# Performance work log

Measured on AMD Instinct MI355X. Metric: run time of the kernel, lower is better.

Reference implementation:

```python
import jax, jax.numpy as jnp
import numpy as np

# longformer-base-4096 config
L, H, D, DH, FF = 12, 12, 768, 64, 3072
B, S, W = 1, 4096, 256            # W = one-sided attention window (attention_window 512)
V, MAXP, NCLS = 50265, 4098, 6
NC = S // W                        # number of chunks of size W


def layer_norm(x, s, b, eps=1e-5):
    m = jnp.mean(x, -1, keepdims=True)
    v = jnp.var(x, -1, keepdims=True)
    return (x - m) * jax.lax.rsqrt(v + eps) * s + b


def sliding_attn(q, k, v, kv_mask):
    # q,k,v: [B,H,S,DH]; kv_mask: [B,S] float (1=keep, 0=pad)
    qc = q.reshape(B, H, NC, W, DH)
    pad = ((0, 0), (0, 0), (W, W), (0, 0))
    kp = jnp.pad(k, pad).reshape(B, H, NC + 2, W, DH)
    vp = jnp.pad(v, pad).reshape(B, H, NC + 2, W, DH)
    # each chunk c sees key chunks c-1, c, c+1 -> [B,H,NC,3W,DH]
    k3 = jnp.concatenate([kp[:, :, i:i + NC] for i in range(3)], axis=3)
    v3 = jnp.concatenate([vp[:, :, i:i + NC] for i in range(3)], axis=3)
    scores = jnp.einsum('bhcqd,bhckd->bhcqk', qc, k3) / np.float32(np.sqrt(DH))
    # banded mask: |key_global - query_global| <= W  <=>  qi <= kj <= qi + 2W
    qi = jnp.arange(W)[:, None]
    kj = jnp.arange(3 * W)[None, :]
    band = (kj >= qi) & (kj <= qi + 2 * W)                       # [W,3W]
    mp = jnp.pad(kv_mask, ((0, 0), (W, W))).reshape(B, NC + 2, W)
    m3 = jnp.concatenate([mp[:, i:i + NC] for i in range(3)], axis=2)  # [B,NC,3W]
    allowed = band[None, None, None] & (m3[:, None, :, None, :] > 0)
    probs = jax.nn.softmax(jnp.where(allowed, scores, -1e9), axis=-1)
    out = jnp.einsum('bhcqk,bhckd->bhcqd', probs, v3)            # [B,H,NC,W,DH]
    return out.reshape(B, H, S, DH)


def setup_inputs():
    ki = iter(jax.random.split(jax.random.key(0), 16))
    p = lambda sh: 0.02 * jax.random.normal(next(ki), sh, jnp.float32)
    ids = jax.random.randint(next(ki), (B, S), 0, V, dtype=jnp.int32)
    mask = jnp.ones((B, S), jnp.int32)
    return dict(
        ids=ids, mask=mask,
        word_emb=p((V, D)), pos_emb=p((MAXP, D)), type_emb=p((D,)),
        ln_e_s=jnp.ones((D,), jnp.float32), ln_e_b=jnp.zeros((D,), jnp.float32),
        wq=p((L, D, D)), bq=jnp.zeros((L, D), jnp.float32),
        wk=p((L, D, D)), bk=jnp.zeros((L, D), jnp.float32),
        wv=p((L, D, D)), bv=jnp.zeros((L, D), jnp.float32),
        wo=p((L, D, D)), bo=jnp.zeros((L, D), jnp.float32),
        ln1_s=jnp.ones((L, D), jnp.float32), ln1_b=jnp.zeros((L, D), jnp.float32),
        w1=p((L, D, FF)), b1=jnp.zeros((L, FF), jnp.float32),
        w2=p((L, FF, D)), b2=jnp.zeros((L, D), jnp.float32),
        ln2_s=jnp.ones((L, D), jnp.float32), ln2_b=jnp.zeros((L, D), jnp.float32),
        w_pool=p((D, D)), b_pool=jnp.zeros((D,), jnp.float32),
        w_cls=p((D, NCLS)), b_cls=jnp.zeros((NCLS,), jnp.float32))


def reference(ids, mask, word_emb, pos_emb, type_emb, ln_e_s, ln_e_b,
              wq, bq, wk, bk, wv, bv, wo, bo, ln1_s, ln1_b,
              w1, b1, w2, b2, ln2_s, ln2_b, w_pool, b_pool, w_cls, b_cls):
    maskf = mask.astype(jnp.float32)
    # RoBERTa-style position ids with padding_idx=1
    pos = (jnp.cumsum(mask, axis=1) * mask + 1).astype(jnp.int32)
    x = word_emb[ids] + pos_emb[pos] + type_emb               # [B,S,D]
    x = layer_norm(x, ln_e_s, ln_e_b)

    def heads(y, w, b):
        return (y @ w + b).reshape(B, S, H, DH).transpose(0, 2, 1, 3)

    for l in range(L):
        q = heads(x, wq[l], bq[l])
        k = heads(x, wk[l], bk[l])
        v = heads(x, wv[l], bv[l])
        a = sliding_attn(q, k, v, maskf)                      # [B,H,S,DH]
        a = a.transpose(0, 2, 1, 3).reshape(B, S, D)
        x = layer_norm(x + (a @ wo[l] + bo[l]), ln1_s[l], ln1_b[l])
        h = jax.nn.gelu(x @ w1[l] + b1[l], approximate=False)
        x = layer_norm(x + (h @ w2[l] + b2[l]), ln2_s[l], ln2_b[l])

    pooled = jnp.tanh(x[:, 0] @ w_pool + b_pool)              # [B,D] pooler
    # Dropout(0.3) is identity in eval mode
    return pooled @ w_cls + b_cls                             # [B,6]
```

## Files before the change

kernel.cpp:

```cpp
#include <hip/hip_runtime.h>
#include <stdint.h>
#include <math.h>

#define NL 12
#define SQ 4096
#define DM 768
#define NH 12
#define DHD 64
#define FF 3072
#define WW 256

typedef unsigned short u16;
typedef __attribute__((ext_vector_type(8))) short bf8_t;
typedef __attribute__((ext_vector_type(4))) short s16x4;
typedef __attribute__((ext_vector_type(4))) float f4;

__device__ __forceinline__ float bf2f(u16 h) {
  union { unsigned int u; float f; } c; c.u = ((unsigned int)h) << 16; return c.f;
}
__device__ __forceinline__ u16 f2bf(float f) {
  union { float f; unsigned int u; } c; c.f = f; unsigned int u = c.u;
  return (u16)((u + 0x7fffu + ((u >> 16) & 1u)) >> 16);
}
__device__ __forceinline__ int iclamp(int v, int lo, int hi) {
  return v < lo ? lo : (v > hi ? hi : v);
}
__device__ __forceinline__ void gload16(const void* g, void* l) {
  __builtin_amdgcn_global_load_lds(
      (const __attribute__((address_space(1))) void*)g,
      (__attribute__((address_space(3))) void*)l, 16, 0, 0);
}

__global__ __launch_bounds__(256) void scan_kernel(const int* __restrict__ mask,
                                                   int* __restrict__ pos) {
  __shared__ int part[256];
  int tid = threadIdx.x;
  int base = tid * 16, ssum = 0;
  for (int i = 0; i < 16; ++i) ssum += mask[base + i];
  part[tid] = ssum;
  __syncthreads();
  if (tid == 0) {
    int run = 0;
    for (int i = 0; i < 256; ++i) { int t = part[i]; part[i] = run; run += t; }
  }
  __syncthreads();
  int run = part[tid];
  for (int i = 0; i < 16; ++i) {
    int m = mask[base + i];
    run += m;
    pos[base + i] = run * m + 1;
  }
}

__device__ __forceinline__ void block_ln4(int row, f4 a, bool act,
    const float* __restrict__ s, const float* __restrict__ b,
    float* __restrict__ xo, u16* __restrict__ xh, float* red, int tid) {
  float s1 = 0.f, s2 = 0.f;
  if (act) {
#pragma unroll
    for (int j = 0; j < 4; ++j) { s1 += a[j]; s2 += a[j] * a[j]; }
  }
#pragma unroll
  for (int m = 1; m < 64; m <<= 1) { s1 += __shfl_xor(s1, m); s2 += __shfl_xor(s2, m); }
  if ((tid & 63) == 0) { red[tid >> 6] = s1; red[4 + (tid >> 6)] = s2; }
  __syncthreads();
  s1 = red[0] + red[1] + red[2] + red[3];
  s2 = red[4] + red[5] + red[6] + red[7];
  float mean = s1 * (1.f / DM);
  float var = s2 * (1.f / DM) - mean * mean;
  float inv = rsqrtf(var + 1e-5f);
  if (act) {
    const f4 sv = ((const f4*)s)[tid];
    const f4 bv = ((const f4*)b)[tid];
    f4 y;
    s16x4 hh;
#pragma unroll
    for (int j = 0; j < 4; ++j) {
      y[j] = (a[j] - mean) * inv * sv[j] + bv[j];
      hh[j] = (short)f2bf(y[j]);
    }
    ((f4*)xo)[(size_t)row * 192 + tid] = y;
    *(s16x4*)&xh[(size_t)row * DM + tid * 4] = hh;
  }
}

__global__ __launch_bounds__(256) void embed_kernel(const int* __restrict__ ids,
    const int* __restrict__ pos, const float* __restrict__ we,
    const float* __restrict__ pe, const float* __restrict__ te,
    const float* __restrict__ s, const float* __restrict__ b,
    float* __restrict__ xo, u16* __restrict__ xh) {
  __shared__ float red[8];
  int row = blockIdx.x, tid = threadIdx.x;
  bool act = tid < 192;
  f4 a = { 0.f, 0.f, 0.f, 0.f };
  if (act) {
    int id = ids[row], pz = pos[row];
    const f4 wv = ((const f4*)we)[(size_t)id * 192 + tid];
    const f4 pv = ((const f4*)pe)[(size_t)pz * 192 + tid];
    const f4 tv = ((const f4*)te)[tid];
#pragma unroll
    for (int j = 0; j < 4; ++j) a[j] = wv[j] + pv[j] + tv[j];
  }
  block_ln4(row, a, act, s, b, xo, xh, red, tid);
}

__global__ __launch_bounds__(256) void ln_direct_kernel(
    const float* __restrict__ in, float* __restrict__ x, u16* __restrict__ xh,
    const float* __restrict__ s, const float* __restrict__ b) {
  __shared__ float red[8];
  int row = blockIdx.x, tid = threadIdx.x;
  bool act = tid < 192;
  f4 a = { 0.f, 0.f, 0.f, 0.f };
  if (act) a = ((const f4*)in)[(size_t)row * 192 + tid];
  block_ln4(row, a, act, s, b, x, xh, red, tid);
}

__global__ __launch_bounds__(256) void ln_fuse_kernel(
    const float* __restrict__ pp, int nparts, const float* __restrict__ bias,
    float* __restrict__ x, u16* __restrict__ xh,
    const float* __restrict__ s, const float* __restrict__ b) {
  __shared__ float red[8];
  int row = blockIdx.x, tid = threadIdx.x;
  bool act = tid < 192;
  f4 a = { 0.f, 0.f, 0.f, 0.f };
  if (act) {
    size_t i4 = (size_t)row * 192 + tid;
    a = ((const f4*)x)[i4];
    const f4 bb = ((const f4*)bias)[tid];
#pragma unroll
    for (int j = 0; j < 4; ++j) a[j] += bb[j];
    for (int p = 0; p < nparts; ++p) {
      const f4 pv = ((const f4*)pp)[(size_t)p * SQ * 192 + i4];
#pragma unroll
      for (int j = 0; j < 4; ++j) a[j] += pv[j];
    }
  }
  block_ln4(row, a, act, s, b, x, xh, red, tid);
}

__global__ __launch_bounds__(256) void wconv_all(
    const float* __restrict__ wq, const float* __restrict__ wk,
    const float* __restrict__ wv, const float* __restrict__ wo,
    const float* __restrict__ w1, const float* __restrict__ w2,
    u16* __restrict__ Wqkv, u16* __restrict__ Wo,
    u16* __restrict__ W1, u16* __restrict__ W2) {
  __shared__ float t[64 * 65];
  int b = blockIdx.x;
  int lay = blockIdx.y;
  const float* src;
  u16* dst;
  int K, N, rowoff, nx, tile;
  if (b < 216) {
    int j = b / 72;
    tile = b - j * 72;
    src = ((j == 0) ? wq : ((j == 1) ? wk : wv)) + (size_t)lay * DM * DM;
    dst = Wqkv + (size_t)lay * 3 * DM * DM;
    K = DM; N = DM; rowoff = j * DM; nx = 12;
  } else if (b < 288) {
    tile = b - 216;
    src = wo + (size_t)lay * DM * DM; dst = Wo + (size_t)lay * DM * DM;
    K = DM; N = DM; rowoff = 0; nx = 12;
  } else if (b < 576) {
    tile = b - 288;
    src = w1 + (size_t)lay * DM * FF; dst = W1 + (size_t)lay * DM * FF;
    K = DM; N = FF; rowoff = 0; nx = 48;
  } else {
    tile = b - 576;
    src = w2 + (size_t)lay * FF * DM; dst = W2 + (size_t)lay * FF * DM;
    K = FF; N = DM; rowoff = 0; nx = 12;
  }
  int n0 = (tile % nx) * 64, k0 = (tile / nx) * 128;
  int tid = threadIdx.x;
  int q = tid & 15, kr = tid >> 4;

  f4 v0[4], v1[4];
#pragma unroll
  for (int p = 0; p < 4; ++p)
    v0[p] = *(const f4*)&src[(size_t)(k0 + kr + p * 16) * N + n0 + q * 4];
#pragma unroll
  for (int p = 0; p < 4; ++p)
    v1[p] = *(const f4*)&src[(size_t)(k0 + 64 + kr + p * 16) * N + n0 + q * 4];

#pragma unroll
  for (int p = 0; p < 4; ++p) {
    int k = kr + p * 16;
#pragma unroll
    for (int j = 0; j < 4; ++j) t[k * 65 + q * 4 + j] = v0[p][j];
  }
  __syncthreads();
  {
    int n = tid >> 4, kq = (tid & 15) * 4;
#pragma unroll
    for (int c = 0; c < 4; ++c) {
      int nn = n + c * 16;
      s16x4 st;
#pragma unroll
      for (int i = 0; i < 4; ++i)
        st[i] = (short)f2bf(t[(kq + i) * 65 + nn]);
      *(s16x4*)&dst[(size_t)(rowoff + n0 + nn) * K + k0 + kq] = st;
    }
  }
  __syncthreads();
#pragma unroll
  for (int p = 0; p < 4; ++p) {
    int k = kr + p * 16;
#pragma unroll
    for (int j = 0; j < 4; ++j) t[k * 65 + q * 4 + j] = v1[p][j];
  }
  __syncthreads();
  {
    int n = tid >> 4, kq = (tid & 15) * 4;
#pragma unroll
    for (int c = 0; c < 4; ++c) {
      int nn = n + c * 16;
      s16x4 st;
#pragma unroll
      for (int i = 0; i < 4; ++i)
        st[i] = (short)f2bf(t[(kq + i) * 65 + nn]);
      *(s16x4*)&dst[(size_t)(rowoff + n0 + nn) * K + k0 + 64 + kq] = st;
    }
  }
}

template <int EPI>
__global__ __launch_bounds__(256, 3) void gemm1(
    const u16* __restrict__ A, const u16* __restrict__ B, int Kld, int ksl,
    int nx, int ntiles,
    const float* __restrict__ bias0, const float* __restrict__ bias1,
    const float* __restrict__ bias2, const float* __restrict__ resid,
    float* __restrict__ outf, u16* __restrict__ oh,
    u16* __restrict__ Qb, u16* __restrict__ Kb, u16* __restrict__ VTb) {
  __shared__ __align__(16) char smem[49152];

  const int tid = threadIdx.x;
  const int l = tid & 63;
  const int w = tid >> 6;
  const int lr = l & 15;
  const int lg = l >> 4;
  const int nwg = gridDim.x;
  const int bid = blockIdx.x;
  const int wg = (bid & 7) * (nwg >> 3) + (bid >> 3);
  const int part = wg / ntiles;
  const int t = wg - part * ntiles;
  const int bm = (t / nx) * 128;
  const int bn = (t % nx) * 64;
  const int k0 = part * ksl;
  const int wr = (w >> 1) * 64;
  const int wc = (w & 1) * 32;

  f4 acc[4][2];
  f4 z = { 0.f, 0.f, 0.f, 0.f };
#pragma unroll
  for (int i = 0; i < 4; ++i)
#pragma unroll
    for (int j = 0; j < 2; ++j) acc[i][j] = z;

  const int srow = tid >> 3;
  const int scol = ((tid & 7) * 8) ^ ((srow & 7) * 8);
  const int xw = (lr & 7) * 8;

  const int nkt = ksl >> 6;

  auto stage = [&](int slot, int kt) {
    int ksrc = k0 + (kt << 6);
    char* la = smem + slot * 24576 + (size_t)(tid & ~63) * 16;
    char* lb = la + 16384;
#pragma unroll
    for (int r = 0; r < 4; ++r)
      gload16(A + (size_t)(bm + srow + r * 32) * Kld + ksrc + scol, la + r * 4096);
#pragma unroll
    for (int r = 0; r < 2; ++r)
      gload16(B + (size_t)(bn + srow + r * 32) * Kld + ksrc + scol, lb + r * 4096);
  };

  stage(0, 0);
  stage(1, 1);
  asm volatile("s_waitcnt vmcnt(6)" ::: "memory");
  __builtin_amdgcn_s_barrier();
  __builtin_amdgcn_sched_barrier(0);

  for (int kt = 0; kt < nkt; ++kt) {
    const int cur = kt & 1;
    const u16* sA = (const u16*)(smem + cur * 24576);
    const u16* sB = sA + 8192;
#pragma unroll
    for (int ks = 0; ks < 2; ++ks) {
      bf8_t af[4], bfr[2];
#pragma unroll
      for (int mt = 0; mt < 4; ++mt)
        af[mt] = *(const bf8_t*)&sA[(wr + mt * 16 + lr) * 64 + ((ks * 32 + lg * 8) ^ xw)];
#pragma unroll
      for (int nt = 0; nt < 2; ++nt)
        bfr[nt] = *(const bf8_t*)&sB[(wc + nt * 16 + lr) * 64 + ((ks * 32 + lg * 8) ^ xw)];
#pragma unroll
      for (int mt = 0; mt < 4; ++mt)
#pragma unroll
        for (int nt = 0; nt < 2; ++nt)
          acc[mt][nt] = __builtin_amdgcn_mfma_f32_16x16x32_bf16(af[mt], bfr[nt], acc[mt][nt], 0, 0, 0);
    }
    asm volatile("s_waitcnt lgkmcnt(0)" ::: "memory");
    __builtin_amdgcn_sched_barrier(0);
    __builtin_amdgcn_s_barrier();
    if (kt + 2 < nkt) {
      stage(cur, kt + 2);
      asm volatile("s_waitcnt vmcnt(6)" ::: "memory");
    } else {
      asm volatile("s_waitcnt vmcnt(0)" ::: "memory");
    }
    __builtin_amdgcn_s_barrier();
    __builtin_amdgcn_sched_barrier(0);
  }
  __syncthreads();

  if constexpr (EPI == 3 || EPI == 4) {
#pragma unroll
    for (int mt = 0; mt < 4; ++mt)
#pragma unroll
      for (int nt = 0; nt < 2; ++nt) {
        int colg = bn + wc + nt * 16 + lr;
#pragma unroll
        for (int r = 0; r < 4; ++r) {
          int rowg = bm + wr + mt * 16 + lg * 4 + r;
          size_t idx = (size_t)rowg * DM + colg;
          if constexpr (EPI == 3) {
            outf[(size_t)part * SQ * DM + idx] = acc[mt][nt][r];
          } else {
            outf[idx] = acc[mt][nt][r] + bias0[colg] + resid[idx];
          }
        }
      }
    return;
  }

  float* ep = (float*)(smem + w * 9216);
  const int nbase = bn + wc;

  if constexpr (EPI == 0) {
    int tgt = nbase / DM;
    int within = nbase - tgt * DM;
    int head = within >> 6;
    const float* bp = (tgt == 0) ? bias0 : ((tgt == 1) ? bias1 : bias2);
    if (tgt == 2) {
#pragma unroll
      for (int mt = 0; mt < 4; ++mt)
#pragma unroll
        for (int nt = 0; nt < 2; ++nt) {
          int dh = (within & 63) + nt * 16 + lr;
          float bb = bp[within + nt * 16 + lr];
          int s0 = bm + wr + mt * 16 + lg * 4;
          s16x4 st;
#pragma unroll
          for (int r = 0; r < 4; ++r) st[r] = (short)f2bf(acc[mt][nt][r] + bb);
          *(s16x4*)&VTb[((size_t)(head * DHD + dh)) * SQ + s0] = st;
        }
    } else {
      u16* dst = (tgt == 0) ? Qb : Kb;
      float scale = (tgt == 0) ? 0.125f : 1.0f;
#pragma unroll
      for (int mt = 0; mt < 4; ++mt)
#pragma unroll
        for (int nt = 0; nt < 2; ++nt)
#pragma unroll
          for (int r = 0; r < 4; ++r)
            ep[(mt * 16 + lg * 4 + r) * 36 + nt * 16 + lr] = acc[mt][nt][r];
      asm volatile("s_waitcnt lgkmcnt(0)" ::: "memory");
      int coloff = (l & 7) * 4;
#pragma unroll
      for (int i = 0; i < 8; ++i) {
        int row = (l >> 3) + i * 8;
        int gs = bm + wr + row;
        f4 v = *(f4*)&ep[row * 36 + coloff];
        s16x4 st;
#pragma unroll
        for (int j = 0; j < 4; ++j)
          st[j] = (short)f2bf((v[j] + bp[within + coloff + j]) * scale);
        *(s16x4*)&dst[((size_t)head * SQ + gs) * DHD + (within & 63) + coloff] = st;
      }
    }
  } else {
#pragma unroll
    for (int mt = 0; mt < 4; ++mt)
#pragma unroll
      for (int nt = 0; nt < 2; ++nt)
#pragma unroll
        for (int r = 0; r < 4; ++r)
          ep[(mt * 16 + lg * 4 + r) * 36 + nt * 16 + lr] = acc[mt][nt][r];
    asm volatile("s_waitcnt lgkmcnt(0)" ::: "memory");
    int coloff = (l & 7) * 4;
#pragma unroll
    for (int i = 0; i < 8; ++i) {
      int row = (l >> 3) + i * 8;
      int gs = bm + wr + row;
      f4 v = *(f4*)&ep[row * 36 + coloff];
      s16x4 hi;
#pragma unroll
      for (int j = 0; j < 4; ++j) {
        float t2 = v[j] + bias0[nbase + coloff + j];
        t2 = 0.5f * t2 * (1.f + erff(t2 * 0.70710678118654752f));
        hi[j] = (short)f2bf(t2);
      }
      *(s16x4*)&oh[(size_t)gs * FF + nbase + coloff] = hi;
    }
  }
}

__global__ __launch_bounds__(64) void attn_kernel(
    const u16* __restrict__ Qb, const u16* __restrict__ Kb,
    const u16* __restrict__ VTb, const int* __restrict__ mask,
    u16* __restrict__ ah) {
  __shared__ __align__(16) u16 Pl[64 * 72];
  __shared__ float mwin[576];
  const int l = threadIdx.x;
  const int lr = l & 15, lg = l >> 4;
  const int h = blockIdx.y;
  const int q0 = blockIdx.x * 64;
  const int kb = q0 - 256;
  for (int i = l; i < 576; i += 64) {
    int kg = kb + i;
    mwin[i] = (kg >= 0 && kg < SQ && mask[kg] != 0) ? 1.f : 0.f;
  }
  __syncthreads();

  bf8_t qf[4][2];
#pragma unroll
  for (int mt = 0; mt < 4; ++mt)
#pragma unroll
    for (int ks = 0; ks < 2; ++ks)
      qf[mt][ks] = *(const bf8_t*)&Qb[((size_t)h * SQ + q0 + mt * 16 + lr) * DHD + ks * 32 + lg * 8];

  f4 o[4][4];
  f4 z = { 0.f, 0.f, 0.f, 0.f };
  float mrow[4][4], lrow[4][4];
#pragma unroll
  for (int mt = 0; mt < 4; ++mt)
#pragma unroll
    for (int nt = 0; nt < 4; ++nt) o[mt][nt] = z;
#pragma unroll
  for (int mt = 0; mt < 4; ++mt)
#pragma unroll
    for (int r = 0; r < 4; ++r) { mrow[mt][r] = -1e30f; lrow[mt][r] = 0.f; }

  for (int kc = 0; kc < 9; ++kc) {
    int klb = kc * 64;
    f4 sc[4][4];
#pragma unroll
    for (int mt = 0; mt < 4; ++mt)
#pragma unroll
      for (int nt = 0; nt < 4; ++nt) sc[mt][nt] = z;
#pragma unroll
    for (int ks = 0; ks < 2; ++ks) {
      bf8_t kf[4];
#pragma unroll
      for (int nt = 0; nt < 4; ++nt) {
        int krow = iclamp(kb + klb + nt * 16 + lr, 0, SQ - 1);
        kf[nt] = *(const bf8_t*)&Kb[((size_t)h * SQ + krow) * DHD + ks * 32 + lg * 8];
      }
#pragma unroll
      for (int mt = 0; mt < 4; ++mt)
#pragma unroll
        for (int nt = 0; nt < 4; ++nt)
          sc[mt][nt] = __builtin_amdgcn_mfma_f32_16x16x32_bf16(qf[mt][ks], kf[nt], sc[mt][nt], 0, 0, 0);
    }
    bool edge = (kc == 0) | (kc == 8);
#pragma unroll
    for (int mt = 0; mt < 4; ++mt)
#pragma unroll
      for (int nt = 0; nt < 4; ++nt) {
        int col = nt * 16 + lr;
        int kg = kb + klb + col;
        float mk = mwin[klb + col];
#pragma unroll
        for (int r = 0; r < 4; ++r) {
          int qg = q0 + mt * 16 + lg * 4 + r;
          int d = kg - qg;
          bool ok = (mk > 0.5f) && (!edge || ((d <= WW) && (d >= -WW)));
          sc[mt][nt][r] = ok ? sc[mt][nt][r] : -3.0e38f;
        }
      }
#pragma unroll
    for (int mt = 0; mt < 4; ++mt)
#pragma unroll
      for (int r = 0; r < 4; ++r) {
        float cm = fmaxf(fmaxf(sc[mt][0][r], sc[mt][1][r]),
                         fmaxf(sc[mt][2][r], sc[mt][3][r]));
#pragma unroll
        for (int m2 = 1; m2 < 16; m2 <<= 1) cm = fmaxf(cm, __shfl_xor(cm, m2));
        float mn = fmaxf(fmaxf(mrow[mt][r], cm), -1e30f);
        float scl = __expf(mrow[mt][r] - mn);
        mrow[mt][r] = mn;
        float ps = 0.f;
#pragma unroll
        for (int nt = 0; nt < 4; ++nt) {
          float pv = __expf(sc[mt][nt][r] - mn);
          sc[mt][nt][r] = pv;
          ps += pv;
        }
#pragma unroll
        for (int m2 = 1; m2 < 16; m2 <<= 1) ps += __shfl_xor(ps, m2);
        lrow[mt][r] = lrow[mt][r] * scl + ps;
#pragma unroll
        for (int nt = 0; nt < 4; ++nt) o[mt][nt][r] *= scl;
#pragma unroll
        for (int nt = 0; nt < 4; ++nt)
          Pl[(mt * 16 + lg * 4 + r) * 72 + nt * 16 + lr] = f2bf(sc[mt][nt][r]);
      }
    asm volatile("s_waitcnt lgkmcnt(0)" ::: "memory");
#pragma unroll
    for (int ks = 0; ks < 2; ++ks) {
      bf8_t pa[4], vf[4];
#pragma unroll
      for (int mt = 0; mt < 4; ++mt)
        pa[mt] = *(const bf8_t*)&Pl[(mt * 16 + lr) * 72 + ks * 32 + lg * 8];
      int kbase = iclamp(kb + klb + ks * 32 + lg * 8, 0, SQ - 8);
#pragma unroll
      for (int nt = 0; nt < 4; ++nt)
        vf[nt] = *(const bf8_t*)&VTb[((size_t)h * DHD + nt * 16 + lr) * SQ + kbase];
#pragma unroll
      for (int mt = 0; mt < 4; ++mt)
#pragma unroll
        for (int nt = 0; nt < 4; ++nt)
          o[mt][nt] = __builtin_amdgcn_mfma_f32_16x16x32_bf16(pa[mt], vf[nt], o[mt][nt], 0, 0, 0);
    }
  }
#pragma unroll
  for (int mt = 0; mt < 4; ++mt)
#pragma unroll
    for (int nt = 0; nt < 4; ++nt) {
      int col = h * DHD + nt * 16 + lr;
#pragma unroll
      for (int r = 0; r < 4; ++r) {
        int gq = q0 + mt * 16 + lg * 4 + r;
        float v = o[mt][nt][r] / lrow[mt][r];
        ah[(size_t)gq * DM + col] = f2bf(v);
      }
    }
}

__global__ __launch_bounds__(256) void head1_kernel(const float* __restrict__ x,
    const float* __restrict__ wp, const float* __restrict__ bp,
    float* __restrict__ y) {
  __shared__ float x0[DM];
  __shared__ float part[4][64];
  int tid = threadIdx.x;
  int w = tid >> 6, l = tid & 63;
  for (int i = tid; i < DM; i += 256) x0[i] = x[i];
  __syncthreads();
  int j = blockIdx.x * 64 + l;
  float a = 0.f;
  int i0 = w * 192;
#pragma unroll 4
  for (int i = i0; i < i0 + 192; ++i) a += x0[i] * wp[(size_t)i * DM + j];
  part[w][l] = a;
  __syncthreads();
  if (w == 0) {
    float t = part[0][l] + part[1][l] + part[2][l] + part[3][l] + bp[j];
    y[j] = tanhf(t);
  }
}

__global__ __launch_bounds__(64) void head2_kernel(const float* __restrict__ y,
    const float* __restrict__ wc, const float* __restrict__ bc,
    float* __restrict__ out) {
  int l = threadIdx.x;
  float acc[6] = {0.f, 0.f, 0.f, 0.f, 0.f, 0.f};
  for (int i = l; i < DM; i += 64) {
    float yv = y[i];
#pragma unroll
    for (int j = 0; j < 6; ++j) acc[j] += yv * wc[i * 6 + j];
  }
#pragma unroll
  for (int j = 0; j < 6; ++j)
#pragma unroll
    for (int m = 1; m < 64; m <<= 1) acc[j] += __shfl_xor(acc[j], m);
  if (l == 0) {
#pragma unroll
    for (int j = 0; j < 6; ++j) out[j] = acc[j] + bc[j];
  }
}

extern "C" void kernel_launch(void* const* d_in, const int* in_sizes, int n_in,
                              void* d_out, int out_size, void* d_ws, size_t ws_size,
                              hipStream_t stream) {
  const int* ids = (const int*)d_in[0];
  const int* mask = (const int*)d_in[1];
  const float* we = (const float*)d_in[2];
  const float* pe = (const float*)d_in[3];
  const float* te = (const float*)d_in[4];
  const float* ln_e_s = (const float*)d_in[5];
  const float* ln_e_b = (const float*)d_in[6];
  const float* wq = (const float*)d_in[7];
  const float* bq = (const float*)d_in[8];
  const float* wk = (const float*)d_in[9];
  const float* bk = (const float*)d_in[10];
  const float* wv = (const float*)d_in[11];
  const float* bv = (const float*)d_in[12];
  const float* wo = (const float*)d_in[13];
  const float* bo = (const float*)d_in[14];
  const float* ln1_s = (const float*)d_in[15];
  const float* ln1_b = (const float*)d_in[16];
  const float* w1 = (const float*)d_in[17];
  const float* b1 = (const float*)d_in[18];
  const float* w2 = (const float*)d_in[19];
  const float* b2 = (const float*)d_in[20];
  const float* ln2_s = (const float*)d_in[21];
  const float* ln2_b = (const float*)d_in[22];
  const float* wpool = (const float*)d_in[23];
  const float* bpool = (const float*)d_in[24];
  const float* wcls = (const float*)d_in[25];
  const float* bcls = (const float*)d_in[26];

  char* p = (char*)d_ws;
  auto take = [&](size_t bytes) {
    char* r = p;
    p += (bytes + 255) & ~(size_t)255;
    return r;
  };
  int* pos = (int*)take((size_t)SQ * 4);
  float* x = (float*)take((size_t)SQ * DM * 4);
  float* pp = (float*)take((size_t)2 * SQ * DM * 4);
  u16* xh = (u16*)take((size_t)SQ * DM * 2);
  u16* Wqkv_h = (u16*)take((size_t)NL * 3 * DM * DM * 2);
  u16* Wo_h = (u16*)take((size_t)NL * DM * DM * 2);
  u16* W1_h = (u16*)take((size_t)NL * DM * FF * 2);
  u16* W2_h = (u16*)take((size_t)NL * FF * DM * 2);
  u16* Qb = (u16*)take((size_t)NH * SQ * DHD * 2);
  u16* Kbf = (u16*)take((size_t)NH * SQ * DHD * 2);
  u16* VTb = (u16*)take((size_t)NH * DHD * SQ * 2);
  u16* ah_ = (u16*)take((size_t)SQ * DM * 2);
  u16* hh = (u16*)take((size_t)SQ * FF * 2);
  float* ypool = (float*)take((size_t)DM * 4);

  scan_kernel<<<dim3(1), dim3(256), 0, stream>>>(mask, pos);
  embed_kernel<<<dim3(SQ), dim3(256), 0, stream>>>(ids, pos, we, pe, te, ln_e_s, ln_e_b, x, xh);
  wconv_all<<<dim3(864, NL), dim3(256), 0, stream>>>(
      wq, wk, wv, wo, w1, w2, Wqkv_h, Wo_h, W1_h, W2_h);

  for (int l = 0; l < NL; ++l) {
    const u16* Wq_l = Wqkv_h + (size_t)l * 3 * DM * DM;
    const u16* Wo_l = Wo_h + (size_t)l * DM * DM;
    const u16* W1_l = W1_h + (size_t)l * DM * FF;
    const u16* W2_l = W2_h + (size_t)l * FF * DM;

    gemm1<0><<<dim3(1152), dim3(256), 0, stream>>>(
        xh, Wq_l, DM, DM, 36, 1152, bq + (size_t)l * DM, bk + (size_t)l * DM,
        bv + (size_t)l * DM, nullptr, nullptr, nullptr, Qb, Kbf, VTb);
    attn_kernel<<<dim3(SQ / 64, NH), dim3(64), 0, stream>>>(Qb, Kbf, VTb, mask, ah_);
    gemm1<4><<<dim3(384), dim3(256), 0, stream>>>(
        ah_, Wo_l, DM, DM, 12, 384, bo + (size_t)l * DM, nullptr, nullptr, x,
        pp, nullptr, nullptr, nullptr, nullptr);
    ln_direct_kernel<<<dim3(SQ), dim3(256), 0, stream>>>(
        pp, x, xh, ln1_s + (size_t)l * DM, ln1_b + (size_t)l * DM);
    gemm1<2><<<dim3(1536), dim3(256), 0, stream>>>(
        xh, W1_l, DM, DM, 48, 1536, b1 + (size_t)l * FF, nullptr, nullptr, nullptr,
        nullptr, hh, nullptr, nullptr, nullptr);
    gemm1<3><<<dim3(768), dim3(256), 0, stream>>>(
        hh, W2_l, FF, FF / 2, 12, 384, nullptr, nullptr, nullptr, nullptr,
        pp, nullptr, nullptr, nullptr, nullptr);
    ln_fuse_kernel<<<dim3(SQ), dim3(256), 0, stream>>>(
        pp, 2, b2 + (size_t)l * DM, x, xh, ln2_s + (size_t)l * DM, ln2_b + (size_t)l * DM);
  }

  head1_kernel<<<dim3(12), dim3(256), 0, stream>>>(x, wpool, bpool, ypool);
  head2_kernel<<<dim3(1), dim3(64), 0, stream>>>(ypool, wcls, bcls, (float*)d_out);
}
```

Before: 2.239 ms.

## Split attention block into two waves of 32 queries and skip mask when fully valid

The attention kernel now launches 128 threads per block, and each of the two waves handles 32 query rows over its own 576-key window. Each wave has a private P staging buffer in LDS, and the mask window is widened to 640 entries. Per-wave register use drops (accumulators and scores are halved), and a ballot over the mask window lets non-edge chunks skip the per-element masking when every key is valid. In exchange, each wave loads its own K/V tiles, so global and L2 traffic for K and V roughly doubles, and the MFMA work per key load goes down.

```diff
diff --git a/kernel.cpp b/kernel.cpp
--- a/kernel.cpp
+++ b/kernel.cpp
@@ -404,47 +404,52 @@
   }
 }
 
-__global__ __launch_bounds__(64) void attn_kernel(
+__global__ __launch_bounds__(128) void attn_kernel(
     const u16* __restrict__ Qb, const u16* __restrict__ Kb,
     const u16* __restrict__ VTb, const int* __restrict__ mask,
     u16* __restrict__ ah) {
-  __shared__ __align__(16) u16 Pl[64 * 72];
-  __shared__ float mwin[576];
-  const int l = threadIdx.x;
+  __shared__ __align__(16) u16 Pl[2][32 * 72];
+  __shared__ float mwin[640];
+  const int tid = threadIdx.x;
+  const int w = tid >> 6;
+  const int l = tid & 63;
   const int lr = l & 15, lg = l >> 4;
   const int h = blockIdx.y;
   const int q0 = blockIdx.x * 64;
-  const int kb = q0 - 256;
-  for (int i = l; i < 576; i += 64) {
-    int kg = kb + i;
+  const int qw = q0 + w * 32;
+  const int kbw = qw - 256;
+  for (int i = tid; i < 640; i += 128) {
+    int kg = q0 - 256 + i;
     mwin[i] = (kg >= 0 && kg < SQ && mask[kg] != 0) ? 1.f : 0.f;
   }
   __syncthreads();
-
-  bf8_t qf[4][2];
-#pragma unroll
-  for (int mt = 0; mt < 4; ++mt)
+  u16* Plw = Pl[w];
+
+  bf8_t qf[2][2];
+#pragma unroll
+  for (int mt = 0; mt < 2; ++mt)
 #pragma unroll
     for (int ks = 0; ks < 2; ++ks)
-      qf[mt][ks] = *(const bf8_t*)&Qb[((size_t)h * SQ + q0 + mt * 16 + lr) * DHD + ks * 32 + lg * 8];
-
-  f4 o[4][4];
+      qf[mt][ks] = *(const bf8_t*)&Qb[((size_t)h * SQ + qw + mt * 16 + lr) * DHD + ks * 32 + lg * 8];
+
+  f4 o[2][4];
   f4 z = { 0.f, 0.f, 0.f, 0.f };
-  float mrow[4][4], lrow[4][4];
-#pragma unroll
-  for (int mt = 0; mt < 4; ++mt)
+  float mrow[2][4], lrow[2][4];
+#pragma unroll
+  for (int mt = 0; mt < 2; ++mt)
 #pragma unroll
     for (int nt = 0; nt < 4; ++nt) o[mt][nt] = z;
 #pragma unroll
-  for (int mt = 0; mt < 4; ++mt)
+  for (int mt = 0; mt < 2; ++mt)
 #pragma unroll
     for (int r = 0; r < 4; ++r) { mrow[mt][r] = -1e30f; lrow[mt][r] = 0.f; }
 
   for (int kc = 0; kc < 9; ++kc) {
     int klb = kc * 64;
-    f4 sc[4][4];
-#pragma unroll
-    for (int mt = 0; mt < 4; ++mt)
+    int mo = w * 32 + klb;
+    f4 sc[2][4];
+#pragma unroll
+    for (int mt = 0; mt < 2; ++mt)
 #pragma unroll
       for (int nt = 0; nt < 4; ++nt) sc[mt][nt] = z;
 #pragma unroll
@@ -452,33 +457,36 @@
       bf8_t kf[4];
 #pragma unroll
       for (int nt = 0; nt < 4; ++nt) {
-        int krow = iclamp(kb + klb + nt * 16 + lr, 0, SQ - 1);
+        int krow = iclamp(kbw + klb + nt * 16 + lr, 0, SQ - 1);
         kf[nt] = *(const bf8_t*)&Kb[((size_t)h * SQ + krow) * DHD + ks * 32 + lg * 8];
       }
 #pragma unroll
-      for (int mt = 0; mt < 4; ++mt)
+      for (int mt = 0; mt < 2; ++mt)
 #pragma unroll
         for (int nt = 0; nt < 4; ++nt)
           sc[mt][nt] = __builtin_amdgcn_mfma_f32_16x16x32_bf16(qf[mt][ks], kf[nt], sc[mt][nt], 0, 0, 0);
     }
     bool edge = (kc == 0) | (kc == 8);
-#pragma unroll
-    for (int mt = 0; mt < 4; ++mt)
-#pragma unroll
-      for (int nt = 0; nt < 4; ++nt) {
-        int col = nt * 16 + lr;
-        int kg = kb + klb + col;
-        float mk = mwin[klb + col];
-#pragma unroll
-        for (int r = 0; r < 4; ++r) {
-          int qg = q0 + mt * 16 + lg * 4 + r;
-          int d = kg - qg;
-          bool ok = (mk > 0.5f) && (!edge || ((d <= WW) && (d >= -WW)));
-          sc[mt][nt][r] = ok ? sc[mt][nt][r] : -3.0e38f;
+    unsigned long long vb = __ballot(mwin[mo + l] > 0.5f);
+    if (edge || vb != ~0ull) {
+#pragma unroll
+      for (int mt = 0; mt < 2; ++mt)
+#pragma unroll
+        for (int nt = 0; nt < 4; ++nt) {
+          int col = nt * 16 + lr;
+          int kg = kbw + klb + col;
+          float mk = mwin[mo + col];
+#pragma unroll
+          for (int r = 0; r < 4; ++r) {
+            int qg = qw + mt * 16 + lg * 4 + r;
+            int d = kg - qg;
+            bool ok = (mk > 0.5f) && (!edge || ((d <= WW) && (d >= -WW)));
+            sc[mt][nt][r] = ok ? sc[mt][nt][r] : -3.0e38f;
+          }
         }
-      }
-#pragma unroll
-    for (int mt = 0; mt < 4; ++mt)
+    }
+#pragma unroll
+    for (int mt = 0; mt < 2; ++mt)
 #pragma unroll
       for (int r = 0; r < 4; ++r) {
         float cm = fmaxf(fmaxf(sc[mt][0][r], sc[mt][1][r]),
@@ -502,34 +510,34 @@
         for (int nt = 0; nt < 4; ++nt) o[mt][nt][r] *= scl;
 #pragma unroll
         for (int nt = 0; nt < 4; ++nt)
-          Pl[(mt * 16 + lg * 4 + r) * 72 + nt * 16 + lr] = f2bf(sc[mt][nt][r]);
+          Plw[(mt * 16 + lg * 4 + r) * 72 + nt * 16 + lr] = f2bf(sc[mt][nt][r]);
       }
     asm volatile("s_waitcnt lgkmcnt(0)" ::: "memory");
 #pragma unroll
     for (int ks = 0; ks < 2; ++ks) {
-      bf8_t pa[4], vf[4];
-#pragma unroll
-      for (int mt = 0; mt < 4; ++mt)
-        pa[mt] = *(const bf8_t*)&Pl[(mt * 16 + lr) * 72 + ks * 32 + lg * 8];
-      int kbase = iclamp(kb + klb + ks * 32 + lg * 8, 0, SQ - 8);
+      bf8_t pa[2], vf[4];
+#pragma unroll
+      for (int mt = 0; mt < 2; ++mt)
+        pa[mt] = *(const bf8_t*)&Plw[(mt * 16 + lr) * 72 + ks * 32 + lg * 8];
+      int kbase = iclamp(kbw + klb + ks * 32 + lg * 8, 0, SQ - 8);
 #pragma unroll
       for (int nt = 0; nt < 4; ++nt)
         vf[nt] = *(const bf8_t*)&VTb[((size_t)h * DHD + nt * 16 + lr) * SQ + kbase];
 #pragma unroll
-      for (int mt = 0; mt < 4; ++mt)
+      for (int mt = 0; mt < 2; ++mt)
 #pragma unroll
         for (int nt = 0; nt < 4; ++nt)
           o[mt][nt] = __builtin_amdgcn_mfma_f32_16x16x32_bf16(pa[mt], vf[nt], o[mt][nt], 0, 0, 0);
     }
   }
 #pragma unroll
-  for (int mt = 0; mt < 4; ++mt)
+  for (int mt = 0; mt < 2; ++mt)
 #pragma unroll
     for (int nt = 0; nt < 4; ++nt) {
       int col = h * DHD + nt * 16 + lr;
 #pragma unroll
       for (int r = 0; r < 4; ++r) {
-        int gq = q0 + mt * 16 + lg * 4 + r;
+        int gq = qw + mt * 16 + lg * 4 + r;
         float v = o[mt][nt][r] / lrow[mt][r];
         ah[(size_t)gq * DM + col] = f2bf(v);
       }
@@ -644,7 +652,7 @@
     gemm1<0><<<dim3(1152), dim3(256), 0, stream>>>(
         xh, Wq_l, DM, DM, 36, 1152, bq + (size_t)l * DM, bk + (size_t)l * DM,
         bv + (size_t)l * DM, nullptr, nullptr, nullptr, Qb, Kbf, VTb);
-    attn_kernel<<<dim3(SQ / 64, NH), dim3(64), 0, stream>>>(Qb, Kbf, VTb, mask, ah_);
+    attn_kernel<<<dim3(SQ / 64, NH), dim3(128), 0, stream>>>(Qb, Kbf, VTb, mask, ah_);
     gemm1<4><<<dim3(384), dim3(256), 0, stream>>>(
         ah_, Wo_l, DM, DM, 12, 384, bo + (size_t)l * DM, nullptr, nullptr, x,
         pp, nullptr, nullptr, nullptr, nullptr);
```

Result: faster. 2.181 ms (-2.6%).
